# Kernel optimization log

Hardware: AMD Instinct MI355X
Metric: run time of the kernel (lower is better)

Reference implementation:

```python
import jax, jax.numpy as jnp
import numpy as np

B, L, H, NH, NB = 4, 200, 256, 4, 2
HS = H // NH
NEG = -(2.0 ** 32) + 1.0  # torch uses (-2**32 + 1) as mask fill
EPS = 1e-8


def _ln(x, g, b):
    m = x.mean(-1, keepdims=True)
    v = ((x - m) ** 2).mean(-1, keepdims=True)
    return (x - m) / jnp.sqrt(v + EPS) * g + b


def _split_heads(x):  # [B,L,H] -> (NH,B,L,HS), matches torch split(dim=2)+cat(dim=0)
    return x.reshape(x.shape[0], x.shape[1], NH, HS).transpose(2, 0, 1, 3)


def _split_heads4(x):  # [B,L,L,H] -> (NH,B,L,L,HS)
    return x.reshape(B, L, L, NH, HS).transpose(3, 0, 1, 2, 4)


def setup_inputs() -> dict:
    key = jax.random.key(0)
    ks = jax.random.split(key, 20)
    w = 0.05
    inp = {
        "log_seqs": jax.random.randint(ks[0], (B, L), 0, 50000),
        "time_matrices": jax.random.randint(ks[1], (B, L, L), 0, 257),
        "dis_matrices": jax.random.randint(ks[2], (B, L, L), 0, 257),
        "item_embs": jax.random.normal(ks[3], (50001, H), jnp.float32) * w,
        "pos_K_tab": jax.random.normal(ks[4], (L, H), jnp.float32) * w,
        "pos_V_tab": jax.random.normal(ks[5], (L, H), jnp.float32) * w,
        "time_K_tab": jax.random.normal(ks[6], (257, H), jnp.float32) * w,
        "time_V_tab": jax.random.normal(ks[7], (257, H), jnp.float32) * w,
        "dis_K_tab": jax.random.normal(ks[8], (257, H), jnp.float32) * w,
        "dis_V_tab": jax.random.normal(ks[9], (257, H), jnp.float32) * w,
        "ln1_g": jnp.ones((NB, H), jnp.float32),
        "ln1_b": jnp.zeros((NB, H), jnp.float32),
        "Wq": jax.random.normal(ks[10], (NB, H, H), jnp.float32) * w,
        "bq": jnp.zeros((NB, H), jnp.float32),
        "Wk": jax.random.normal(ks[11], (NB, H, H), jnp.float32) * w,
        "bk": jnp.zeros((NB, H), jnp.float32),
        "Wv": jax.random.normal(ks[12], (NB, H, H), jnp.float32) * w,
        "bv": jnp.zeros((NB, H), jnp.float32),
        "ln2_g": jnp.ones((NB, H), jnp.float32),
        "ln2_b": jnp.zeros((NB, H), jnp.float32),
        "W1": jax.random.normal(ks[13], (NB, H, H), jnp.float32) * w,
        "b1": jnp.zeros((NB, H), jnp.float32),
        "W2": jax.random.normal(ks[14], (NB, H, H), jnp.float32) * w,
        "b2": jnp.zeros((NB, H), jnp.float32),
        "lnf_g": jnp.ones((H,), jnp.float32),
        "lnf_b": jnp.zeros((H,), jnp.float32),
    }
    return inp


def _seq2feats(log_seqs, time_matrices, dis_matrices, item_embs,
               pos_K_tab, pos_V_tab, time_K_tab, time_V_tab, dis_K_tab, dis_V_tab,
               ln1_g, ln1_b, Wq, bq, Wk, bk, Wv, bv,
               ln2_g, ln2_b, W1, b1, W2, b2, lnf_g, lnf_b):
    # embedded relative matrices: (NH,B,L,L,HS)
    tK = _split_heads4(time_K_tab[time_matrices])
    tV = _split_heads4(time_V_tab[time_matrices])
    dK = _split_heads4(dis_K_tab[dis_matrices])
    dV = _split_heads4(dis_V_tab[dis_matrices])
    pK = pos_K_tab.reshape(L, NH, HS).transpose(1, 0, 2)  # (NH,L,HS), same for every batch row
    pV = pos_V_tab.reshape(L, NH, HS).transpose(1, 0, 2)

    pad = (log_seqs == 0)  # [B,L]
    keep = (~pad)[..., None].astype(jnp.float32)
    seqs = item_embs[log_seqs] * keep

    causal = ~jnp.tril(jnp.ones((L, L), dtype=bool))  # strictly upper
    mask = pad[None, :, :, None] | causal[None, None, :, :]  # (1,B,L,L) broadcast over heads
    scale = jnp.sqrt(jnp.float32(HS))

    for i in range(NB):
        Qn = _ln(seqs, ln1_g[i], ln1_b[i])
        Qh = _split_heads(Qn @ Wq[i].T + bq[i])
        Kh = _split_heads(seqs @ Wk[i].T + bk[i])
        Vh = _split_heads(seqs @ Wv[i].T + bv[i])
        s = (jnp.einsum('hbqd,hbkd->hbqk', Qh, Kh)
             + jnp.einsum('hbqd,hkd->hbqk', Qh, pK)
             + jnp.einsum('hbqkd,hbqd->hbqk', tK, Qh)
             + jnp.einsum('hbqkd,hbqd->hbqk', dK, Qh)) / scale
        s = jnp.where(mask, NEG, s)
        A = jax.nn.softmax(s, axis=-1)  # (NH,B,L,L)
        o = (jnp.einsum('hbqk,hbkd->hbqd', A, Vh)
             + jnp.einsum('hbqk,hkd->hbqd', A, pV)
             + jnp.einsum('hbqk,hbqkd->hbqd', A, tV)
             + jnp.einsum('hbqk,hbqkd->hbqd', A, dV))
        mha = o.transpose(1, 2, 0, 3).reshape(B, L, H)
        seqs = Qn + mha
        x = _ln(seqs, ln2_g[i], ln2_b[i])
        h = jax.nn.relu(x @ W1[i].T + b1[i])  # Conv1d k=1 == pointwise linear
        seqs = (h @ W2[i].T + b2[i]) + x
        seqs = seqs * keep
    return _ln(seqs, lnf_g, lnf_b)


def reference(log_seqs, time_matrices, dis_matrices, item_embs,
              pos_K_tab, pos_V_tab, time_K_tab, time_V_tab, dis_K_tab, dis_V_tab,
              ln1_g, ln1_b, Wq, bq, Wk, bk, Wv, bv,
              ln2_g, ln2_b, W1, b1, W2, b2, lnf_g, lnf_b):
    return _seq2feats(log_seqs, time_matrices, dis_matrices, item_embs,
                      pos_K_tab, pos_V_tab, time_K_tab, time_V_tab, dis_K_tab, dis_V_tab,
                      ln1_g, ln1_b, Wq, bq, Wk, bk, Wv, bv,
                      ln2_g, ln2_b, W1, b1, W2, b2, lnf_g, lnf_b)
```

## Files before the change

### kernel.cpp

```cpp
#include <hip/hip_runtime.h>
#include <math.h>

typedef __fp16 h2 __attribute__((ext_vector_type(2)));
typedef __fp16 f16x8 __attribute__((ext_vector_type(8)));
typedef float f32x4 __attribute__((ext_vector_type(4)));

#define Bc 4
#define Lc 200
#define Hc 256
#define NHc 4
#define HSc 64
#define NBc 2
#define Mtot (Bc*Lc)
#define TROW 34
#define LDH 264
#define WN (2*Hc*Hc)
#define TN (257*Hc)

static __device__ __forceinline__ float neg_fill() { return -4294967295.0f; }
static __device__ __forceinline__ int rl(int x) { return __builtin_amdgcn_readfirstlane(x); }

static __device__ __forceinline__ uint pkh2(float a, float b) {
  h2 r = __builtin_amdgcn_cvt_pkrtz(a, b);
  return __builtin_bit_cast(uint, r);
}
static __device__ __forceinline__ h2 u2h(uint u) { return __builtin_bit_cast(h2, u); }
static __device__ __forceinline__ float h2f(ushort u) {
  return (float)__builtin_bit_cast(_Float16, u);
}

__global__ void cvtw_k(const float* __restrict__ Wq, const float* __restrict__ Wk,
                       const float* __restrict__ Wv, const float* __restrict__ W1,
                       const float* __restrict__ W2,
                       const float* __restrict__ tK, const float* __restrict__ tV,
                       const float* __restrict__ dK, const float* __restrict__ dV,
                       ushort* __restrict__ out) {
  int y = blockIdx.y;
  const float* src;
  int n, off;
  if (y < 5) {
    n = WN; off = y * WN;
    src = (y == 0) ? Wq : (y == 1) ? Wk : (y == 2) ? Wv : (y == 3) ? W1 : W2;
  } else {
    n = TN; off = 5 * WN + (y - 5) * TN;
    src = (y == 5) ? tK : (y == 6) ? tV : (y == 7) ? dK : dV;
  }
  int idx = (blockIdx.x * 256 + threadIdx.x) * 8;
  if (idx >= n) return;
  float4 a = *(const float4*)&src[idx];
  float4 b = *(const float4*)&src[idx + 4];
  uint4 o;
  o.x = pkh2(a.x, a.y); o.y = pkh2(a.z, a.w);
  o.z = pkh2(b.x, b.y); o.w = pkh2(b.z, b.w);
  *(uint4*)&out[off + idx] = o;
}

__global__ __launch_bounds__(256)
void mmqkv_k(const float* __restrict__ seqs, const float* __restrict__ emb,
             const int* __restrict__ logs, int useEmb,
             const float* __restrict__ g, const float* __restrict__ bt,
             const ushort* __restrict__ Wq16, const ushort* __restrict__ Wk16,
             const ushort* __restrict__ Wv16,
             const float* __restrict__ bq, const float* __restrict__ bk,
             const float* __restrict__ bv,
             const float* __restrict__ pK, const float* __restrict__ pV,
             float* __restrict__ Qn,
             ushort* __restrict__ Q16, ushort* __restrict__ K16,
             ushort* __restrict__ V16) {
  __shared__ __fp16 Al[16][LDH];
  __shared__ __fp16 Wl[64][LDH];
  int m0 = blockIdx.x * 16;
  int y = blockIdx.y;
  int region = y >> 2, nloc = (y & 3) * 64;
  const ushort* Wsrc = (region == 0) ? Wq16 : (region == 1 ? Wk16 : Wv16);
  const float* bias = (region == 0) ? bq : (region == 1 ? bk : bv);
  int t = threadIdx.x;
  if (region == 0) {
    int r = t >> 4, c0 = (t & 15) * 16;
    int m = m0 + r;
    const float* xr;
    bool zero = false;
    if (useEmb) {
      int tok = logs[m];
      zero = (tok == 0);
      xr = &emb[tok * Hc + c0];
    } else {
      xr = &seqs[m * Hc + c0];
    }
    float4 v0, v1, v2, v3;
    if (zero) {
      v0 = v1 = v2 = v3 = make_float4(0.f, 0.f, 0.f, 0.f);
    } else {
      v0 = *(const float4*)&xr[0];
      v1 = *(const float4*)&xr[4];
      v2 = *(const float4*)&xr[8];
      v3 = *(const float4*)&xr[12];
    }
    float s = v0.x + v0.y + v0.z + v0.w + v1.x + v1.y + v1.z + v1.w
            + v2.x + v2.y + v2.z + v2.w + v3.x + v3.y + v3.z + v3.w;
    float q = v0.x*v0.x + v0.y*v0.y + v0.z*v0.z + v0.w*v0.w
            + v1.x*v1.x + v1.y*v1.y + v1.z*v1.z + v1.w*v1.w
            + v2.x*v2.x + v2.y*v2.y + v2.z*v2.z + v2.w*v2.w
            + v3.x*v3.x + v3.y*v3.y + v3.z*v3.z + v3.w*v3.w;
#pragma unroll
    for (int o = 1; o < 16; o <<= 1) { s += __shfl_xor(s, o); q += __shfl_xor(q, o); }
    float mean = s * (1.f / Hc);
    float var = q * (1.f / Hc) - mean * mean;
    float rstd = 1.f / sqrtf(var + 1e-8f);
    float tmp[16] = {v0.x,v0.y,v0.z,v0.w,v1.x,v1.y,v1.z,v1.w,
                     v2.x,v2.y,v2.z,v2.w,v3.x,v3.y,v3.z,v3.w};
    float nv[16];
#pragma unroll
    for (int j = 0; j < 16; ++j)
      nv[j] = (tmp[j] - mean) * rstd * g[c0 + j] + bt[c0 + j];
#pragma unroll
    for (int j = 0; j < 16; j += 2)
      *(h2*)&Al[r][c0 + j] = __builtin_amdgcn_cvt_pkrtz(nv[j], nv[j + 1]);
    if (y == 0) {
#pragma unroll
      for (int j = 0; j < 16; j += 4)
        *(float4*)&Qn[m * Hc + c0 + j] = make_float4(nv[j], nv[j+1], nv[j+2], nv[j+3]);
    }
  } else {
    for (int i = t; i < 16 * 64; i += 256) {
      int r = i >> 6, c = (i & 63) * 4;
      int m = m0 + r;
      float4 v;
      if (useEmb) {
        int tok = logs[m];
        v = (tok == 0) ? make_float4(0.f, 0.f, 0.f, 0.f)
                       : *(const float4*)&emb[tok * Hc + c];
      } else {
        v = *(const float4*)&seqs[m * Hc + c];
      }
      *(h2*)&Al[r][c] = __builtin_amdgcn_cvt_pkrtz(v.x, v.y);
      *(h2*)&Al[r][c + 2] = __builtin_amdgcn_cvt_pkrtz(v.z, v.w);
    }
  }
  for (int i = t; i < 2048; i += 256) {
    int r = i >> 5, c = (i & 31) * 8;
    uint4 v = *(const uint4*)&Wsrc[(nloc + r) * Hc + c];
    *(uint4*)&Wl[r][c] = v;
  }
  __syncthreads();
  int wave = t >> 6, lane = t & 63;
  int row = lane & 15, kg = lane >> 4;
  int bn = wave * 16 + row;
  f32x4 acc = {0.f, 0.f, 0.f, 0.f};
#pragma unroll
  for (int k0 = 0; k0 < Hc; k0 += 32) {
    int kk = k0 + kg * 8;
    f16x8 a = *(const f16x8*)&Al[row][kk];
    f16x8 bb = *(const f16x8*)&Wl[bn][kk];
    acc = __builtin_amdgcn_mfma_f32_16x16x32_f16(a, bb, acc, 0, 0, 0);
  }
  int coln = nloc + wave * 16 + row;
  ushort* op = (region == 0) ? Q16 : (region == 1 ? K16 : V16);
  const float* pT = (region == 1) ? pK : pV;
#pragma unroll
  for (int r = 0; r < 4; ++r) {
    int m = m0 + kg * 4 + r;
    float v = acc[r] + bias[coln];
    if (region) v += pT[(m % Lc) * Hc + coln];
    op[m * Hc + coln] = __builtin_bit_cast(ushort, (_Float16)v);
  }
}

__global__ __launch_bounds__(1024, 4)
void attn_k(const ushort* __restrict__ Q16, const ushort* __restrict__ K16,
            const ushort* __restrict__ V16,
            const ushort* __restrict__ tK16, const ushort* __restrict__ dK16,
            const ushort* __restrict__ tV16, const ushort* __restrict__ dV16,
            const int* __restrict__ tm, const int* __restrict__ dm,
            const int* __restrict__ logs,
            const float* __restrict__ Qn, float* __restrict__ seqs) {
  int h = blockIdx.x, b = blockIdx.y, bz = blockIdx.z;
  __shared__ uint tVs[257 * TROW];
  __shared__ uint dVs[257 * TROW];
  __shared__ float S0l[16][212];
  __shared__ float Tql[16][272];
  __shared__ float Dql[16][272];
  __shared__ float sArow[16][204];
  int t = threadIdx.x;
  int wave = t >> 6, lane = t & 63;
  int row16 = lane & 15, kg = lane >> 4;
  {
    const ushort* s1 = tV16 + h * HSc;
    const ushort* s2 = dV16 + h * HSc;
    for (int i = t; i < 257 * 8; i += 1024) {
      int r = i >> 3, c = (i & 7) * 8;
      *(uint4*)&tVs[r * TROW + (c >> 1)] = *(const uint4*)&s1[r * Hc + c];
      *(uint4*)&dVs[r * TROW + (c >> 1)] = *(const uint4*)&s2[r * Hc + c];
    }
  }
  {
    int qa = row16 * 16 + bz;
    bool va = qa < Lc;
    f16x8 A0 = {0,0,0,0,0,0,0,0}, A1 = A0;
    if (va) {
      const ushort* Qr = &Q16[(b * Lc + qa) * Hc + h * HSc];
      A0 = *(const f16x8*)&Qr[kg * 8];
      A1 = *(const f16x8*)&Qr[32 + kg * 8];
    }
    for (int j = wave; j < 47; j += 16) {
      int kind, n;
      if (j < 13) { kind = 0; n = j; }
      else if (j < 30) { kind = 1; n = j - 13; }
      else { kind = 2; n = j - 30; }
      int col = n * 16 + row16;
      const ushort* Bsrc;
      bool vb;
      if (kind == 0) { vb = col < Lc; Bsrc = &K16[(b * Lc + (vb ? col : 0)) * Hc + h * HSc]; }
      else { vb = col < 257; Bsrc = &((kind == 1) ? tK16 : dK16)[(vb ? col : 0) * Hc + h * HSc]; }
      f16x8 B0 = {0,0,0,0,0,0,0,0}, B1 = B0;
      if (vb) {
        B0 = *(const f16x8*)&Bsrc[kg * 8];
        B1 = *(const f16x8*)&Bsrc[32 + kg * 8];
      }
      f32x4 acc = {0.f, 0.f, 0.f, 0.f};
      acc = __builtin_amdgcn_mfma_f32_16x16x32_f16(A0, B0, acc, 0, 0, 0);
      acc = __builtin_amdgcn_mfma_f32_16x16x32_f16(A1, B1, acc, 0, 0, 0);
      if (kind == 0) {
#pragma unroll
        for (int r = 0; r < 4; ++r) S0l[kg * 4 + r][col] = acc[r];
      } else if (kind == 1) {
#pragma unroll
        for (int r = 0; r < 4; ++r) Tql[kg * 4 + r][col] = acc[r];
      } else {
#pragma unroll
        for (int r = 0; r < 4; ++r) Dql[kg * 4 + r][col] = acc[r];
      }
    }
  }
  __syncthreads();
  int q = wave * 16 + bz;
  if (q >= Lc) return;
  int m = b * Lc + q;
  int oi = m * Hc + h * HSc + lane;
  if (logs[m] == 0) { seqs[oi] = Qn[oi]; return; }
  const int* tmr = tm + rl(m * Lc);
  const int* dmr = dm + rl(m * Lc);
  const float* srow = S0l[wave];
  const float* trow = Tql[wave];
  const float* drow = Dql[wave];
  int np = (q >> 6) + 1;
  float sv[4];
  float mx = neg_fill();
#pragma unroll
  for (int p = 0; p < 4; ++p) {
    sv[p] = neg_fill();
    if (p >= np) continue;
    int k = p * 64 + lane;
    int kc = (k <= q) ? k : q;
    int ti = tmr[kc], di = dmr[kc];
    float sc = (srow[kc] + trow[ti] + drow[di]) * 0.125f;
    if (k <= q) sv[p] = sc;
    mx = fmaxf(mx, sv[p]);
  }
#pragma unroll
  for (int o = 32; o; o >>= 1) mx = fmaxf(mx, __shfl_xor(mx, o));
  float sum = 0.f;
  float ev[4];
#pragma unroll
  for (int p = 0; p < 4; ++p) {
    ev[p] = __expf(sv[p] - mx);
    sum += ev[p];
  }
#pragma unroll
  for (int o = 32; o; o >>= 1) sum += __shfl_xor(sum, o);
  float rs = 1.f / sum;
#pragma unroll
  for (int p = 0; p < 4; ++p) {
    if (p >= np) continue;
    int k = p * 64 + lane;
    if (k < Lc) sArow[wave][k] = ev[p] * rs;
  }
  for (int k = q + 1 + lane; k < 204; k += 64) sArow[wave][k] = 0.f;
  int half = lane >> 5, li = lane & 31;
  const uint* Vu = (const uint*)V16 + rl(b * Lc * (Hc / 2) + h * (HSc / 2)) + li;
  float acc0 = 0.f, acc1 = 0.f, acc2 = 0.f, acc3 = 0.f;
  for (int k0 = 0; k0 <= q; k0 += 4) {
    int ka = k0 + half;
    int kb = k0 + 2 + half;
    int kca = (ka <= q) ? ka : q;
    int kcb = (kb <= q) ? kb : q;
    float aa = sArow[wave][ka];
    float ab = sArow[wave][kb];
    int ti0 = tmr[kca], di0 = dmr[kca];
    int ti1 = tmr[kcb], di1 = dmr[kcb];
    uint tv0 = tVs[ti0 * TROW + li];
    uint dv0 = dVs[di0 * TROW + li];
    uint vv0 = Vu[kca * (Hc / 2)];
    uint tv1 = tVs[ti1 * TROW + li];
    uint dv1 = dVs[di1 * TROW + li];
    uint vv1 = Vu[kcb * (Hc / 2)];
    h2 s0 = u2h(tv0) + u2h(dv0) + u2h(vv0);
    h2 s1 = u2h(tv1) + u2h(dv1) + u2h(vv1);
    acc0 = fmaf(aa, (float)s0.x, acc0);
    acc1 = fmaf(aa, (float)s0.y, acc1);
    acc2 = fmaf(ab, (float)s1.x, acc2);
    acc3 = fmaf(ab, (float)s1.y, acc3);
  }
  float accLo = acc0 + acc2; accLo += __shfl_xor(accLo, 32);
  float accHi = acc1 + acc3; accHi += __shfl_xor(accHi, 32);
  if (half == 0) {
    int oib = m * Hc + h * HSc + 2 * li;
    float2 qv = *(const float2*)&Qn[oib];
    float2 r;
    r.x = qv.x + accLo;
    r.y = qv.y + accHi;
    *(float2*)&seqs[oib] = r;
  }
}

template <int FIN>
__global__ __launch_bounds__(512)
void ffn_k(float* __restrict__ seqs,
           const float* __restrict__ g, const float* __restrict__ bt,
           const ushort* __restrict__ W1_16, const float* __restrict__ b1,
           const ushort* __restrict__ W2_16, const float* __restrict__ b2,
           const int* __restrict__ logs,
           const float* __restrict__ lnf_g, const float* __restrict__ lnf_b,
           float* __restrict__ dout) {
  __shared__ __fp16 Xl[16][LDH];
  __shared__ __fp16 Hl[16][LDH];
  __shared__ __fp16 Wl[128][LDH];
  __shared__ float Ol[16][Hc];
  int m0 = blockIdx.x * 16;
  int t = threadIdx.x;
  {
    int r = t >> 5, c0 = (t & 31) * 8;
    const float* xr = &seqs[(m0 + r) * Hc + c0];
    float4 v0 = *(const float4*)&xr[0];
    float4 v1 = *(const float4*)&xr[4];
    float s = v0.x + v0.y + v0.z + v0.w + v1.x + v1.y + v1.z + v1.w;
    float q = v0.x*v0.x + v0.y*v0.y + v0.z*v0.z + v0.w*v0.w
            + v1.x*v1.x + v1.y*v1.y + v1.z*v1.z + v1.w*v1.w;
#pragma unroll
    for (int o = 1; o < 32; o <<= 1) { s += __shfl_xor(s, o); q += __shfl_xor(q, o); }
    float mean = s * (1.f / Hc);
    float var = q * (1.f / Hc) - mean * mean;
    float rstd = 1.f / sqrtf(var + 1e-8f);
    float tmp[8] = {v0.x,v0.y,v0.z,v0.w,v1.x,v1.y,v1.z,v1.w};
    float nv[8];
#pragma unroll
    for (int j = 0; j < 8; ++j)
      nv[j] = (tmp[j] - mean) * rstd * g[c0 + j] + bt[c0 + j];
#pragma unroll
    for (int j = 0; j < 8; j += 2)
      *(h2*)&Xl[r][c0 + j] = __builtin_amdgcn_cvt_pkrtz(nv[j], nv[j + 1]);
  }
  int wave = t >> 6, lane = t & 63;
  int row = lane & 15, kg = lane >> 4;
#pragma unroll
  for (int ch = 0; ch < 2; ++ch) {
    __syncthreads();
    for (int i = t; i < 4096; i += 512) {
      int r = i >> 5, c = (i & 31) * 8;
      uint4 v = *(const uint4*)&W1_16[(ch * 128 + r) * Hc + c];
      *(uint4*)&Wl[r][c] = v;
    }
    __syncthreads();
    int bn = wave * 16 + row;
    f32x4 acc = {0.f, 0.f, 0.f, 0.f};
#pragma unroll
    for (int k0 = 0; k0 < Hc; k0 += 32) {
      int kk = k0 + kg * 8;
      f16x8 a = *(const f16x8*)&Xl[row][kk];
      f16x8 bb = *(const f16x8*)&Wl[bn][kk];
      acc = __builtin_amdgcn_mfma_f32_16x16x32_f16(a, bb, acc, 0, 0, 0);
    }
    int coln = ch * 128 + wave * 16 + row;
    float bv = b1[coln];
#pragma unroll
    for (int r = 0; r < 4; ++r) {
      float v = fmaxf(acc[r] + bv, 0.f);
      Hl[kg * 4 + r][coln] = (_Float16)v;
    }
  }
#pragma unroll
  for (int ch = 0; ch < 2; ++ch) {
    __syncthreads();
    for (int i = t; i < 4096; i += 512) {
      int r = i >> 5, c = (i & 31) * 8;
      uint4 v = *(const uint4*)&W2_16[(ch * 128 + r) * Hc + c];
      *(uint4*)&Wl[r][c] = v;
    }
    __syncthreads();
    int bn = wave * 16 + row;
    f32x4 acc = {0.f, 0.f, 0.f, 0.f};
#pragma unroll
    for (int k0 = 0; k0 < Hc; k0 += 32) {
      int kk = k0 + kg * 8;
      f16x8 a = *(const f16x8*)&Hl[row][kk];
      f16x8 bb = *(const f16x8*)&Wl[bn][kk];
      acc = __builtin_amdgcn_mfma_f32_16x16x32_f16(a, bb, acc, 0, 0, 0);
    }
    int coln = ch * 128 + wave * 16 + row;
    float bv = b2[coln];
#pragma unroll
    for (int r = 0; r < 4; ++r) {
      int mrow = kg * 4 + r;
      int m = m0 + mrow;
      float keep = (logs[m] != 0) ? 1.f : 0.f;
      float xv = h2f(__builtin_bit_cast(ushort, Xl[mrow][coln]));
      float val = (acc[r] + bv + xv) * keep;
      if (FIN) Ol[mrow][coln] = val;
      else     seqs[m * Hc + coln] = val;
    }
  }
  if (FIN) {
    __syncthreads();
    int r = t >> 5, c0 = (t & 31) * 8;
    float v[8];
#pragma unroll
    for (int j = 0; j < 8; ++j) v[j] = Ol[r][c0 + j];
    float s = 0.f, q = 0.f;
#pragma unroll
    for (int j = 0; j < 8; ++j) { s += v[j]; q += v[j] * v[j]; }
#pragma unroll
    for (int o = 1; o < 32; o <<= 1) { s += __shfl_xor(s, o); q += __shfl_xor(q, o); }
    float mean = s * (1.f / Hc);
    float var = q * (1.f / Hc) - mean * mean;
    float rstd = 1.f / sqrtf(var + 1e-8f);
#pragma unroll
    for (int j = 0; j < 8; ++j)
      dout[(m0 + r) * Hc + c0 + j] = (v[j] - mean) * rstd * lnf_g[c0 + j] + lnf_b[c0 + j];
  }
}

extern "C" void kernel_launch(void* const* d_in, const int* in_sizes, int n_in,
                              void* d_out, int out_size, void* d_ws, size_t ws_size,
                              hipStream_t stream) {
  const int* logs = (const int*)d_in[0];
  const int* tm   = (const int*)d_in[1];
  const int* dm   = (const int*)d_in[2];
  const float* item = (const float*)d_in[3];
  const float* pK = (const float*)d_in[4];
  const float* pV = (const float*)d_in[5];
  const float* tK = (const float*)d_in[6];
  const float* tV = (const float*)d_in[7];
  const float* dK = (const float*)d_in[8];
  const float* dV = (const float*)d_in[9];
  const float* ln1_g = (const float*)d_in[10];
  const float* ln1_b = (const float*)d_in[11];
  const float* Wq = (const float*)d_in[12];
  const float* bq = (const float*)d_in[13];
  const float* Wk = (const float*)d_in[14];
  const float* bk = (const float*)d_in[15];
  const float* Wv = (const float*)d_in[16];
  const float* bv = (const float*)d_in[17];
  const float* ln2_g = (const float*)d_in[18];
  const float* ln2_b = (const float*)d_in[19];
  const float* W1 = (const float*)d_in[20];
  const float* b1 = (const float*)d_in[21];
  const float* W2 = (const float*)d_in[22];
  const float* b2 = (const float*)d_in[23];
  const float* lnf_g = (const float*)d_in[24];
  const float* lnf_b = (const float*)d_in[25];

  const int NROW = Mtot * Hc;
  float* ws = (float*)d_ws;
  float* sSeqs = ws + 0 * NROW;
  float* sQn   = ws + 1 * NROW;
  ushort* Q16  = (ushort*)(ws + 2 * NROW);
  ushort* K16  = Q16 + NROW;
  ushort* V16  = K16 + NROW;
  ushort* w16  = (ushort*)(ws + 4 * NROW);
  ushort* wq16 = w16 + 0 * WN;
  ushort* wk16 = w16 + 1 * WN;
  ushort* wv16 = w16 + 2 * WN;
  ushort* w116 = w16 + 3 * WN;
  ushort* w216 = w16 + 4 * WN;
  ushort* tK16 = w16 + 5 * WN;
  ushort* tV16 = tK16 + TN;
  ushort* dK16 = tV16 + TN;
  ushort* dV16 = dK16 + TN;

  dim3 gC(64, 9);
  cvtw_k<<<gC, 256, 0, stream>>>(Wq, Wk, Wv, W1, W2, tK, tV, dK, dV, w16);

  dim3 gQKV(Mtot / 16, 12);
  dim3 ga(NHc, Bc, 16);
  const int HHh = Hc * Hc;
  for (int i = 0; i < NBc; ++i) {
    mmqkv_k<<<gQKV, 256, 0, stream>>>(sSeqs, item, logs, (i == 0) ? 1 : 0,
                                      ln1_g + i * Hc, ln1_b + i * Hc,
                                      wq16 + i * HHh, wk16 + i * HHh, wv16 + i * HHh,
                                      bq + i * Hc, bk + i * Hc, bv + i * Hc,
                                      pK, pV, sQn, Q16, K16, V16);
    attn_k<<<ga, 1024, 0, stream>>>(Q16, K16, V16,
                                    tK16, dK16, tV16, dV16,
                                    tm, dm, logs, sQn, sSeqs);
    if (i == 0)
      ffn_k<0><<<Mtot / 16, 512, 0, stream>>>(sSeqs, ln2_g + i * Hc, ln2_b + i * Hc,
                                              w116 + i * HHh, b1 + i * Hc,
                                              w216 + i * HHh, b2 + i * Hc, logs,
                                              nullptr, nullptr, nullptr);
    else
      ffn_k<1><<<Mtot / 16, 512, 0, stream>>>(sSeqs, ln2_g + i * Hc, ln2_b + i * Hc,
                                              w116 + i * HHh, b1 + i * Hc,
                                              w216 + i * HHh, b2 + i * Hc, logs,
                                              lnf_g, lnf_b, (float*)d_out);
  }
}
```

Before: 75.89 us.

## Double QKV rows per block and read dV table from global in attention

The QKV projection kernel now processes 32 rows per block with two MFMA accumulators sharing one weight fragment, halving the grid and the number of weight tile loads into LDS. The attention kernel stops staging the dV relative-distance table in shared memory and gathers it straight from global memory. It also unrolls the value-accumulation loop by two. The LDS change cuts shared memory use and staging time, which may raise occupancy, but adds scattered global gathers that rely on cache hits.

Result: slower. 84.04 us (+10.7%).

```diff
diff --git a/kernel.cpp b/kernel.cpp
--- a/kernel.cpp
+++ b/kernel.cpp
@@ -67,62 +67,65 @@
              float* __restrict__ Qn,
              ushort* __restrict__ Q16, ushort* __restrict__ K16,
              ushort* __restrict__ V16) {
-  __shared__ __fp16 Al[16][LDH];
+  __shared__ __fp16 Al[32][LDH];
   __shared__ __fp16 Wl[64][LDH];
-  int m0 = blockIdx.x * 16;
+  int m0 = blockIdx.x * 32;
   int y = blockIdx.y;
   int region = y >> 2, nloc = (y & 3) * 64;
   const ushort* Wsrc = (region == 0) ? Wq16 : (region == 1 ? Wk16 : Wv16);
   const float* bias = (region == 0) ? bq : (region == 1 ? bk : bv);
   int t = threadIdx.x;
   if (region == 0) {
-    int r = t >> 4, c0 = (t & 15) * 16;
-    int m = m0 + r;
-    const float* xr;
-    bool zero = false;
-    if (useEmb) {
-      int tok = logs[m];
-      zero = (tok == 0);
-      xr = &emb[tok * Hc + c0];
-    } else {
-      xr = &seqs[m * Hc + c0];
-    }
-    float4 v0, v1, v2, v3;
-    if (zero) {
-      v0 = v1 = v2 = v3 = make_float4(0.f, 0.f, 0.f, 0.f);
-    } else {
-      v0 = *(const float4*)&xr[0];
-      v1 = *(const float4*)&xr[4];
-      v2 = *(const float4*)&xr[8];
-      v3 = *(const float4*)&xr[12];
-    }
-    float s = v0.x + v0.y + v0.z + v0.w + v1.x + v1.y + v1.z + v1.w
-            + v2.x + v2.y + v2.z + v2.w + v3.x + v3.y + v3.z + v3.w;
-    float q = v0.x*v0.x + v0.y*v0.y + v0.z*v0.z + v0.w*v0.w
-            + v1.x*v1.x + v1.y*v1.y + v1.z*v1.z + v1.w*v1.w
-            + v2.x*v2.x + v2.y*v2.y + v2.z*v2.z + v2.w*v2.w
-            + v3.x*v3.x + v3.y*v3.y + v3.z*v3.z + v3.w*v3.w;
-#pragma unroll
-    for (int o = 1; o < 16; o <<= 1) { s += __shfl_xor(s, o); q += __shfl_xor(q, o); }
-    float mean = s * (1.f / Hc);
-    float var = q * (1.f / Hc) - mean * mean;
-    float rstd = 1.f / sqrtf(var + 1e-8f);
-    float tmp[16] = {v0.x,v0.y,v0.z,v0.w,v1.x,v1.y,v1.z,v1.w,
-                     v2.x,v2.y,v2.z,v2.w,v3.x,v3.y,v3.z,v3.w};
-    float nv[16];
-#pragma unroll
-    for (int j = 0; j < 16; ++j)
-      nv[j] = (tmp[j] - mean) * rstd * g[c0 + j] + bt[c0 + j];
-#pragma unroll
-    for (int j = 0; j < 16; j += 2)
-      *(h2*)&Al[r][c0 + j] = __builtin_amdgcn_cvt_pkrtz(nv[j], nv[j + 1]);
-    if (y == 0) {
-#pragma unroll
-      for (int j = 0; j < 16; j += 4)
-        *(float4*)&Qn[m * Hc + c0 + j] = make_float4(nv[j], nv[j+1], nv[j+2], nv[j+3]);
+#pragma unroll
+    for (int hh = 0; hh < 2; ++hh) {
+      int r = hh * 16 + (t >> 4), c0 = (t & 15) * 16;
+      int m = m0 + r;
+      const float* xr;
+      bool zero = false;
+      if (useEmb) {
+        int tok = logs[m];
+        zero = (tok == 0);
+        xr = &emb[tok * Hc + c0];
+      } else {
+        xr = &seqs[m * Hc + c0];
+      }
+      float4 v0, v1, v2, v3;
+      if (zero) {
+        v0 = v1 = v2 = v3 = make_float4(0.f, 0.f, 0.f, 0.f);
+      } else {
+        v0 = *(const float4*)&xr[0];
+        v1 = *(const float4*)&xr[4];
+        v2 = *(const float4*)&xr[8];
+        v3 = *(const float4*)&xr[12];
+      }
+      float s = v0.x + v0.y + v0.z + v0.w + v1.x + v1.y + v1.z + v1.w
+              + v2.x + v2.y + v2.z + v2.w + v3.x + v3.y + v3.z + v3.w;
+      float q = v0.x*v0.x + v0.y*v0.y + v0.z*v0.z + v0.w*v0.w
+              + v1.x*v1.x + v1.y*v1.y + v1.z*v1.z + v1.w*v1.w
+              + v2.x*v2.x + v2.y*v2.y + v2.z*v2.z + v2.w*v2.w
+              + v3.x*v3.x + v3.y*v3.y + v3.z*v3.z + v3.w*v3.w;
+#pragma unroll
+      for (int o = 1; o < 16; o <<= 1) { s += __shfl_xor(s, o); q += __shfl_xor(q, o); }
+      float mean = s * (1.f / Hc);
+      float var = q * (1.f / Hc) - mean * mean;
+      float rstd = 1.f / sqrtf(var + 1e-8f);
+      float tmp[16] = {v0.x,v0.y,v0.z,v0.w,v1.x,v1.y,v1.z,v1.w,
+                       v2.x,v2.y,v2.z,v2.w,v3.x,v3.y,v3.z,v3.w};
+      float nv[16];
+#pragma unroll
+      for (int j = 0; j < 16; ++j)
+        nv[j] = (tmp[j] - mean) * rstd * g[c0 + j] + bt[c0 + j];
+#pragma unroll
+      for (int j = 0; j < 16; j += 2)
+        *(h2*)&Al[r][c0 + j] = __builtin_amdgcn_cvt_pkrtz(nv[j], nv[j + 1]);
+      if (y == 0) {
+#pragma unroll
+        for (int j = 0; j < 16; j += 4)
+          *(float4*)&Qn[m * Hc + c0 + j] = make_float4(nv[j], nv[j+1], nv[j+2], nv[j+3]);
+      }
     }
   } else {
-    for (int i = t; i < 16 * 64; i += 256) {
+    for (int i = t; i < 32 * 64; i += 256) {
       int r = i >> 6, c = (i & 63) * 4;
       int m = m0 + r;
       float4 v;
@@ -146,23 +149,33 @@
   int wave = t >> 6, lane = t & 63;
   int row = lane & 15, kg = lane >> 4;
   int bn = wave * 16 + row;
-  f32x4 acc = {0.f, 0.f, 0.f, 0.f};
+  f32x4 acc0 = {0.f, 0.f, 0.f, 0.f};
+  f32x4 acc1 = {0.f, 0.f, 0.f, 0.f};
 #pragma unroll
   for (int k0 = 0; k0 < Hc; k0 += 32) {
     int kk = k0 + kg * 8;
-    f16x8 a = *(const f16x8*)&Al[row][kk];
     f16x8 bb = *(const f16x8*)&Wl[bn][kk];
-    acc = __builtin_amdgcn_mfma_f32_16x16x32_f16(a, bb, acc, 0, 0, 0);
+    f16x8 a0 = *(const f16x8*)&Al[row][kk];
+    f16x8 a1 = *(const f16x8*)&Al[16 + row][kk];
+    acc0 = __builtin_amdgcn_mfma_f32_16x16x32_f16(a0, bb, acc0, 0, 0, 0);
+    acc1 = __builtin_amdgcn_mfma_f32_16x16x32_f16(a1, bb, acc1, 0, 0, 0);
   }
   int coln = nloc + wave * 16 + row;
   ushort* op = (region == 0) ? Q16 : (region == 1 ? K16 : V16);
   const float* pT = (region == 1) ? pK : pV;
+  float bcol = bias[coln];
 #pragma unroll
   for (int r = 0; r < 4; ++r) {
-    int m = m0 + kg * 4 + r;
-    float v = acc[r] + bias[coln];
-    if (region) v += pT[(m % Lc) * Hc + coln];
-    op[m * Hc + coln] = __builtin_bit_cast(ushort, (_Float16)v);
+    int ma = m0 + kg * 4 + r;
+    int mb = ma + 16;
+    float va = acc0[r] + bcol;
+    float vb = acc1[r] + bcol;
+    if (region) {
+      va += pT[(ma % Lc) * Hc + coln];
+      vb += pT[(mb % Lc) * Hc + coln];
+    }
+    op[ma * Hc + coln] = __builtin_bit_cast(ushort, (_Float16)va);
+    op[mb * Hc + coln] = __builtin_bit_cast(ushort, (_Float16)vb);
   }
 }
 
@@ -176,7 +189,6 @@
             const float* __restrict__ Qn, float* __restrict__ seqs) {
   int h = blockIdx.x, b = blockIdx.y, bz = blockIdx.z;
   __shared__ uint tVs[257 * TROW];
-  __shared__ uint dVs[257 * TROW];
   __shared__ float S0l[16][212];
   __shared__ float Tql[16][272];
   __shared__ float Dql[16][272];
@@ -186,11 +198,9 @@
   int row16 = lane & 15, kg = lane >> 4;
   {
     const ushort* s1 = tV16 + h * HSc;
-    const ushort* s2 = dV16 + h * HSc;
     for (int i = t; i < 257 * 8; i += 1024) {
       int r = i >> 3, c = (i & 7) * 8;
       *(uint4*)&tVs[r * TROW + (c >> 1)] = *(const uint4*)&s1[r * Hc + c];
-      *(uint4*)&dVs[r * TROW + (c >> 1)] = *(const uint4*)&s2[r * Hc + c];
     }
   }
   {
@@ -277,8 +287,10 @@
   }
   for (int k = q + 1 + lane; k < 204; k += 64) sArow[wave][k] = 0.f;
   int half = lane >> 5, li = lane & 31;
-  const uint* Vu = (const uint*)V16 + rl(b * Lc * (Hc / 2) + h * (HSc / 2)) + li;
+  const uint* Vu  = (const uint*)V16 + rl(b * Lc * (Hc / 2) + h * (HSc / 2)) + li;
+  const uint* dVg = (const uint*)dV16 + rl(h * (HSc / 2)) + li;
   float acc0 = 0.f, acc1 = 0.f, acc2 = 0.f, acc3 = 0.f;
+#pragma unroll 2
   for (int k0 = 0; k0 <= q; k0 += 4) {
     int ka = k0 + half;
     int kb = k0 + 2 + half;
@@ -289,10 +301,10 @@
     int ti0 = tmr[kca], di0 = dmr[kca];
     int ti1 = tmr[kcb], di1 = dmr[kcb];
     uint tv0 = tVs[ti0 * TROW + li];
-    uint dv0 = dVs[di0 * TROW + li];
+    uint dv0 = dVg[di0 * (Hc / 2)];
     uint vv0 = Vu[kca * (Hc / 2)];
     uint tv1 = tVs[ti1 * TROW + li];
-    uint dv1 = dVs[di1 * TROW + li];
+    uint dv1 = dVg[di1 * (Hc / 2)];
     uint vv1 = Vu[kcb * (Hc / 2)];
     h2 s0 = u2h(tv0) + u2h(dv0) + u2h(vv0);
     h2 s1 = u2h(tv1) + u2h(dv1) + u2h(vv1);
@@ -480,7 +492,7 @@
   dim3 gC(64, 9);
   cvtw_k<<<gC, 256, 0, stream>>>(Wq, Wk, Wv, W1, W2, tK, tV, dK, dV, w16);
 
-  dim3 gQKV(Mtot / 16, 12);
+  dim3 gQKV(Mtot / 32, 12);
   dim3 ga(NHc, Bc, 16);
   const int HHh = Hc * Hc;
   for (int i = 0; i < NBc; ++i) {
```
